# Kernel tuning notes

Measured on AMD Instinct MI355X. Metric: run time of the kernel, lower is better.

Reference implementation:

```python
import jax, jax.numpy as jnp
import numpy as np

# Router hyperparameters (from init_kwargs)
E = 64        # num_routed_experts
K = 6         # moe_router_topk
G = 8         # num_expert_groups
TG = 3        # topk_group
ALPHA = 0.001 # aux_loss_alpha
EPG = E // G  # experts per group


def setup_inputs() -> dict:
    key = jax.random.key(0)
    k1, k2 = jax.random.split(key)
    hidden_states = jax.random.normal(k1, (4, 4096, 4096), dtype=jnp.float32)
    # kaiming_uniform-ish scale for the gate weight [E, H]
    bound = 1.0 / np.sqrt(4096)
    weight = jax.random.uniform(k2, (E, 4096), dtype=jnp.float32,
                                minval=-bound, maxval=bound)
    return {"hidden_states": hidden_states, "weight": weight}


def reference(hidden_states, weight):
    B, S, H = hidden_states.shape
    T = B * S
    x = hidden_states.reshape(T, H).astype(jnp.float32)
    # gate GEMM + softmax scoring
    logits = jnp.einsum('th,eh->te', x, weight.astype(jnp.float32))  # [T, E]
    scores = jax.nn.softmax(logits, axis=-1)
    # group-limited greedy: keep only experts in the top-TG groups (by group max)
    group_scores = scores.reshape(T, G, EPG).max(axis=-1)            # [T, G]
    _, group_idx = jax.lax.top_k(group_scores, TG)                   # [T, TG]
    group_mask = jnp.zeros((T, G), scores.dtype).at[
        jnp.arange(T)[:, None], group_idx].set(1.0)                  # [T, G]
    score_mask = jnp.repeat(group_mask, EPG, axis=-1)                # [T, E]
    tmp_scores = jnp.where(score_mask > 0, scores, 0.0)
    topk_weight, topk_idx = jax.lax.top_k(tmp_scores, K)             # [T, K]
    # norm_topk_prob = True and top_k > 1 -> normalize
    topk_weight = topk_weight / (topk_weight.sum(axis=-1, keepdims=True) + 1e-20)
    # sequence-level aux loss (seq_aux=True, training, alpha > 0)
    idx_aux = topk_idx.reshape(B, S * K)                             # [B, S*K]
    ce = jax.vmap(lambda idx: jnp.zeros(E, jnp.float32).at[idx].add(1.0))(idx_aux)
    ce = ce / (S * K / E)                                            # [B, E]
    aux_loss = (ce * scores.reshape(B, S, E).mean(axis=1)).sum(axis=1).mean() * ALPHA
    return topk_idx, topk_weight, aux_loss
```

## Files before the change

### kernel.cpp

```cpp
#include <hip/hip_runtime.h>
#include <math.h>

#define TTOK   16384
#define HDIM   4096
#define ENUM   64
#define KTOP   6
#define GNUM   8
#define TGK    3
#define BBATCH 4
#define SSEQ   4096
#define ALPHAC 0.001f

#define KSPLIT 4
#define KSL    (HDIM / KSPLIT)
#define BK     64
#define GNIT   (KSL / BK)

#define AS3(p) ((__attribute__((address_space(3))) void*)(p))
#define AS1(p) ((const __attribute__((address_space(1))) void*)(p))

__global__ __launch_bounds__(256)
void pack_w(const float* __restrict__ W, float* __restrict__ Wp) {
    const int gid = blockIdx.x * 256 + threadIdx.x;
    const int k4 = gid >> 6, e = gid & 63;
    float4 v = *(const float4*)(W + (size_t)e * HDIM + k4 * 4);
    *(float4*)(Wp + (size_t)gid * 4) = v;
}

__global__ __launch_bounds__(512, 4)
void gate_gemm(const float* __restrict__ X, const float* __restrict__ Wp,
               float* __restrict__ lp) {
    __shared__ __align__(16) float Xs[2][64 * 64];

    const int tid = threadIdx.x;
    const int w   = __builtin_amdgcn_readfirstlane(tid >> 6);
    const int l   = tid & 63;
    const int tile  = blockIdx.x & 255;
    const int slice = blockIdx.x >> 8;
    const int tok0  = tile * 64;
    const int k0    = slice * KSL;

    const int t0 = w * 8 + (l >> 4);
    const int t1 = t0 + 4;
    const int q0 = (l & 15) ^ (t0 & 15);
    const int q1 = (l & 15) ^ (t1 & 15);
    const float* g0 = X + (size_t)(tok0 + t0) * HDIM + k0 + q0 * 4;
    const float* g1 = X + (size_t)(tok0 + t1) * HDIM + k0 + q1 * 4;

    float acc[8];
#pragma unroll
    for (int j = 0; j < 8; ++j) acc[j] = 0.f;

    const float4* Wp4 = (const float4*)Wp;
    const int k4base  = k0 >> 2;
    const int w8      = w * 8;
    const int lm      = (l & 15);

    __builtin_amdgcn_global_load_lds(AS1(g0), AS3(&Xs[0][w * 512 + 0]),   16, 0, 0);
    __builtin_amdgcn_global_load_lds(AS1(g1), AS3(&Xs[0][w * 512 + 256]), 16, 0, 0);

    for (int it = 0; it < GNIT; ++it) {
        __syncthreads();
        if (it + 1 < GNIT) {
            const int buf = (it + 1) & 1;
            const size_t go = (size_t)(it + 1) * BK;
            __builtin_amdgcn_global_load_lds(AS1(g0 + go), AS3(&Xs[buf][w * 512 + 0]),   16, 0, 0);
            __builtin_amdgcn_global_load_lds(AS1(g1 + go), AS3(&Xs[buf][w * 512 + 256]), 16, 0, 0);
        }
        const float* xb = &Xs[it & 1][l * 64];
        const int k4it  = k4base + it * 16;
#pragma unroll
        for (int kq = 0; kq < 16; ++kq) {
            const float4 xv = *(const float4*)(xb + ((kq ^ lm) << 2));
            const size_t wb = (size_t)(k4it + kq) * 64 + w8;
#pragma unroll
            for (int j = 0; j < 8; ++j) {
                const float4 wv = Wp4[wb + j];
                acc[j] = fmaf(xv.x, wv.x, acc[j]);
                acc[j] = fmaf(xv.y, wv.y, acc[j]);
                acc[j] = fmaf(xv.z, wv.z, acc[j]);
                acc[j] = fmaf(xv.w, wv.w, acc[j]);
            }
        }
    }

    float* dst = lp + (size_t)slice * TTOK * ENUM + (size_t)(tok0 + l) * ENUM + w8;
    *(float4*)(dst + 0) = make_float4(acc[0], acc[1], acc[2], acc[3]);
    *(float4*)(dst + 4) = make_float4(acc[4], acc[5], acc[6], acc[7]);
}

#define RTOK 64
__global__ __launch_bounds__(256)
void router_topk(const float* __restrict__ lp,
                 float* __restrict__ out_idx, float* __restrict__ out_w,
                 float* __restrict__ ssum_g, int* __restrict__ cnt_g) {
    __shared__ float Ls[RTOK * 67];
    __shared__ float s_m[RTOK], s_inv[RTOK];
    __shared__ float s_ssum[ENUM];
    __shared__ int   s_cnt[ENUM];

    const int tid = threadIdx.x;
    const int t0  = blockIdx.x * RTOK;
    if (tid < ENUM) { s_cnt[tid] = 0; s_ssum[tid] = 0.f; }

#pragma unroll
    for (int r = 0; r < 4; ++r) {
        const int q  = r * 256 + tid;
        const int t  = q >> 4, c4 = q & 15;
        const size_t base = (size_t)(t0 + t) * ENUM + c4 * 4;
        float4 v = *(const float4*)(lp + base);
#pragma unroll
        for (int h = 1; h < KSPLIT; ++h) {
            float4 u = *(const float4*)(lp + (size_t)h * TTOK * ENUM + base);
            v.x += u.x; v.y += u.y; v.z += u.z; v.w += u.w;
        }
        float* d = Ls + t * 67 + c4 * 4;
        d[0] = v.x; d[1] = v.y; d[2] = v.z; d[3] = v.w;
    }
    __syncthreads();

    if (tid < RTOK) {
        const float* row = Ls + tid * 67;

        float gm[GNUM];
#pragma unroll
        for (int g = 0; g < GNUM; ++g) {
            float mg = row[g * 8];
#pragma unroll
            for (int j = 1; j < 8; ++j) mg = fmaxf(mg, row[g * 8 + j]);
            gm[g] = mg;
        }
        float m = gm[0];
#pragma unroll
        for (int g = 1; g < GNUM; ++g) m = fmaxf(m, gm[g]);

        int selmask = 0;
#pragma unroll
        for (int g = 0; g < GNUM; ++g) {
            int rank = 0;
#pragma unroll
            for (int g2 = 0; g2 < GNUM; ++g2)
                rank += (gm[g2] > gm[g]) || (gm[g2] == gm[g] && g2 < g);
            selmask |= (rank < TGK) << g;
        }

        float v0=-1.f,v1=-1.f,v2=-1.f,v3=-1.f,v4=-1.f,v5=-1.f;
        float i0=0.f,i1=0.f,i2=0.f,i3=0.f,i4=0.f,i5=0.f;
        float s = 0.f;
#pragma unroll
        for (int e = 0; e < ENUM; ++e) {
            const float ex = __expf(row[e] - m);
            s += ex;
            const float cand = ((selmask >> (e >> 3)) & 1) ? ex : -1.0f;
            const float fe = (float)e;
            const bool b0 = cand > v0, b1 = cand > v1, b2 = cand > v2,
                       b3 = cand > v3, b4 = cand > v4, b5 = cand > v5;
            v5 = b4 ? v4 : (b5 ? cand : v5);  i5 = b4 ? i4 : (b5 ? fe : i5);
            v4 = b3 ? v3 : (b4 ? cand : v4);  i4 = b3 ? i3 : (b4 ? fe : i4);
            v3 = b2 ? v2 : (b3 ? cand : v3);  i3 = b2 ? i2 : (b3 ? fe : i3);
            v2 = b1 ? v1 : (b2 ? cand : v2);  i2 = b1 ? i1 : (b2 ? fe : i2);
            v1 = b0 ? v0 : (b1 ? cand : v1);  i1 = b0 ? i0 : (b1 ? fe : i1);
            v0 = b0 ? cand : v0;              i0 = b0 ? fe : i0;
        }
        const float invw = 1.0f / (v0 + v1 + v2 + v3 + v4 + v5);
        const int t = t0 + tid;
        float* oi = out_idx + (size_t)t * KTOP;
        float* ow = out_w   + (size_t)t * KTOP;
        oi[0]=i0; oi[1]=i1; oi[2]=i2; oi[3]=i3; oi[4]=i4; oi[5]=i5;
        ow[0]=v0*invw; ow[1]=v1*invw; ow[2]=v2*invw;
        ow[3]=v3*invw; ow[4]=v4*invw; ow[5]=v5*invw;

        atomicAdd(&s_cnt[(int)i0], 1); atomicAdd(&s_cnt[(int)i1], 1);
        atomicAdd(&s_cnt[(int)i2], 1); atomicAdd(&s_cnt[(int)i3], 1);
        atomicAdd(&s_cnt[(int)i4], 1); atomicAdd(&s_cnt[(int)i5], 1);
        s_m[tid] = m; s_inv[tid] = 1.0f / s;
    }
    __syncthreads();

    {
        const int e = tid & 63, strip = tid >> 6;
        float acc = 0.f;
#pragma unroll
        for (int i = 0; i < RTOK / 4; ++i) {
            const int t = strip * (RTOK / 4) + i;
            acc += __expf(Ls[t * 67 + e] - s_m[t]) * s_inv[t];
        }
        atomicAdd(&s_ssum[e], acc);
    }
    __syncthreads();

    const int b = t0 / SSEQ;
    if (tid < ENUM) {
        atomicAdd(&ssum_g[b * ENUM + tid], s_ssum[tid]);
        atomicAdd(&cnt_g[b * ENUM + tid], s_cnt[tid]);
    }
}

__global__ __launch_bounds__(256)
void aux_loss(const float* __restrict__ ssum_g, const int* __restrict__ cnt_g,
              float* __restrict__ out_aux) {
    const int tid = threadIdx.x;
    float v = (float)cnt_g[tid] * (float)ENUM / ((float)SSEQ * (float)KTOP)
            * (ssum_g[tid] / (float)SSEQ);
#pragma unroll
    for (int off = 32; off; off >>= 1) v += __shfl_xor(v, off);
    __shared__ float red[4];
    if ((tid & 63) == 0) red[tid >> 6] = v;
    __syncthreads();
    if (tid == 0)
        out_aux[0] = (red[0] + red[1] + red[2] + red[3]) * (ALPHAC / (float)BBATCH);
}

extern "C" void kernel_launch(void* const* d_in, const int* in_sizes, int n_in,
                              void* d_out, int out_size, void* d_ws, size_t ws_size,
                              hipStream_t stream) {
    const float* X = (const float*)d_in[0];
    const float* W = (const float*)d_in[1];

    float* out     = (float*)d_out;
    float* out_idx = out;
    float* out_w   = out + (size_t)TTOK * KTOP;
    float* out_aux = out + (size_t)2 * TTOK * KTOP;

    float* lp     = (float*)d_ws;
    float* Wp     = lp + (size_t)KSPLIT * TTOK * ENUM;
    float* ssum_g = Wp + (size_t)HDIM * ENUM;
    int*   cnt_g  = (int*)(ssum_g + BBATCH * ENUM);

    hipMemsetAsync(ssum_g, 0, BBATCH * ENUM * (sizeof(float) + sizeof(int)), stream);

    pack_w<<<(HDIM / 4) * ENUM / 256, 256, 0, stream>>>(W, Wp);
    gate_gemm<<<256 * KSPLIT, 512, 0, stream>>>(X, Wp, lp);
    router_topk<<<TTOK / RTOK, 256, 0, stream>>>(lp, out_idx, out_w, ssum_g, cnt_g);
    aux_loss<<<1, 256, 0, stream>>>(ssum_g, cnt_g, out_aux);
}
```

Before: 498.1 us.

## Retile gate GEMM to 256-token by 32-expert blocks with register blocking

Each block of the gate GEMM now covers 256 tokens and half of the experts, with BK set to 32. Each thread accumulates a 4x4 register tile of tokens by experts and loads a 16-float vector of W that is reused across 4 X rows. Blocks are remapped so that related blocks land on the same XCD. This cuts W load traffic per FMA, but X is now read twice from global memory, once per expert half.

```diff
diff --git a/kernel.cpp b/kernel.cpp
--- a/kernel.cpp
+++ b/kernel.cpp
@@ -13,11 +13,15 @@
 
 #define KSPLIT 4
 #define KSL    (HDIM / KSPLIT)
-#define BK     64
-#define GNIT   (KSL / BK)
+#define TM     256
+#define TE     32
+#define BK     32
+#define NIT    (KSL / BK)
 
 #define AS3(p) ((__attribute__((address_space(3))) void*)(p))
 #define AS1(p) ((const __attribute__((address_space(1))) void*)(p))
+
+typedef float wvec16 __attribute__((ext_vector_type(16)));
 
 __global__ __launch_bounds__(256)
 void pack_w(const float* __restrict__ W, float* __restrict__ Wp) {
@@ -30,63 +34,76 @@
 __global__ __launch_bounds__(512, 4)
 void gate_gemm(const float* __restrict__ X, const float* __restrict__ Wp,
                float* __restrict__ lp) {
-    __shared__ __align__(16) float Xs[2][64 * 64];
+    __shared__ __align__(16) float Xs[2][TM * BK];
 
     const int tid = threadIdx.x;
     const int w   = __builtin_amdgcn_readfirstlane(tid >> 6);
     const int l   = tid & 63;
-    const int tile  = blockIdx.x & 255;
-    const int slice = blockIdx.x >> 8;
-    const int tok0  = tile * 64;
-    const int k0    = slice * KSL;
-
-    const int t0 = w * 8 + (l >> 4);
-    const int t1 = t0 + 4;
-    const int q0 = (l & 15) ^ (t0 & 15);
-    const int q1 = (l & 15) ^ (t1 & 15);
-    const float* g0 = X + (size_t)(tok0 + t0) * HDIM + k0 + q0 * 4;
-    const float* g1 = X + (size_t)(tok0 + t1) * HDIM + k0 + q1 * 4;
-
-    float acc[8];
-#pragma unroll
-    for (int j = 0; j < 8; ++j) acc[j] = 0.f;
-
-    const float4* Wp4 = (const float4*)Wp;
-    const int k4base  = k0 >> 2;
-    const int w8      = w * 8;
-    const int lm      = (l & 15);
-
-    __builtin_amdgcn_global_load_lds(AS1(g0), AS3(&Xs[0][w * 512 + 0]),   16, 0, 0);
-    __builtin_amdgcn_global_load_lds(AS1(g1), AS3(&Xs[0][w * 512 + 256]), 16, 0, 0);
-
-    for (int it = 0; it < GNIT; ++it) {
+    const int lm7 = l & 7;
+
+    const int id     = blockIdx.x;
+    const int linear = (id & 7) * 64 + (id >> 3);
+    const int eh     = linear & 1;
+    const int ts     = linear >> 1;
+    const int tile   = ts & 63;
+    const int slice  = ts >> 6;
+    const int T0     = tile * TM;
+    const int k0     = slice * KSL;
+    const int E0     = eh * TE + w * 4;
+
+    const int trow = l >> 3;
+    const int kswz = ((l & 7) ^ trow) << 2;
+    const float* gs = X + (size_t)(T0 + w * 8 + trow) * HDIM + k0 + kswz;
+
+#define STAGE(buf_, it_) do {                                                   \
+    const size_t go_ = (size_t)(it_) * BK;                                      \
+    _Pragma("unroll")                                                           \
+    for (int r_ = 0; r_ < 4; ++r_)                                              \
+        __builtin_amdgcn_global_load_lds(                                       \
+            AS1(gs + (size_t)r_ * 64 * HDIM + go_),                             \
+            AS3(&Xs[buf_][r_ * 2048 + w * 256]), 16, 0, 0);                     \
+} while (0)
+
+    float acc[4][4];
+#pragma unroll
+    for (int g = 0; g < 4; ++g)
+#pragma unroll
+        for (int j = 0; j < 4; ++j) acc[g][j] = 0.f;
+
+    const int k4base = k0 >> 2;
+
+    STAGE(0, 0);
+
+    for (int it = 0; it < NIT; ++it) {
         __syncthreads();
-        if (it + 1 < GNIT) {
-            const int buf = (it + 1) & 1;
-            const size_t go = (size_t)(it + 1) * BK;
-            __builtin_amdgcn_global_load_lds(AS1(g0 + go), AS3(&Xs[buf][w * 512 + 0]),   16, 0, 0);
-            __builtin_amdgcn_global_load_lds(AS1(g1 + go), AS3(&Xs[buf][w * 512 + 256]), 16, 0, 0);
-        }
-        const float* xb = &Xs[it & 1][l * 64];
-        const int k4it  = k4base + it * 16;
-#pragma unroll
-        for (int kq = 0; kq < 16; ++kq) {
-            const float4 xv = *(const float4*)(xb + ((kq ^ lm) << 2));
-            const size_t wb = (size_t)(k4it + kq) * 64 + w8;
-#pragma unroll
-            for (int j = 0; j < 8; ++j) {
-                const float4 wv = Wp4[wb + j];
-                acc[j] = fmaf(xv.x, wv.x, acc[j]);
-                acc[j] = fmaf(xv.y, wv.y, acc[j]);
-                acc[j] = fmaf(xv.z, wv.z, acc[j]);
-                acc[j] = fmaf(xv.w, wv.w, acc[j]);
+        if (it + 1 < NIT) STAGE((it + 1) & 1, it + 1);
+
+        const float* xb = Xs[it & 1];
+        const int k4it  = k4base + it * (BK / 4);
+#pragma unroll
+        for (int kq = 0; kq < 8; ++kq) {
+            const wvec16 wv = *(const wvec16*)(Wp + ((size_t)(k4it + kq) * ENUM + E0) * 4);
+            const int slot = (kq ^ lm7) << 2;
+#pragma unroll
+            for (int g = 0; g < 4; ++g) {
+                const float4 xv = *(const float4*)(xb + (g * 64 + l) * BK + slot);
+#pragma unroll
+                for (int j = 0; j < 4; ++j) {
+                    acc[g][j] = fmaf(xv.x, wv[4 * j + 0], acc[g][j]);
+                    acc[g][j] = fmaf(xv.y, wv[4 * j + 1], acc[g][j]);
+                    acc[g][j] = fmaf(xv.z, wv[4 * j + 2], acc[g][j]);
+                    acc[g][j] = fmaf(xv.w, wv[4 * j + 3], acc[g][j]);
+                }
             }
         }
     }
 
-    float* dst = lp + (size_t)slice * TTOK * ENUM + (size_t)(tok0 + l) * ENUM + w8;
-    *(float4*)(dst + 0) = make_float4(acc[0], acc[1], acc[2], acc[3]);
-    *(float4*)(dst + 4) = make_float4(acc[4], acc[5], acc[6], acc[7]);
+    float* dst = lp + (size_t)slice * TTOK * ENUM + (size_t)(T0 + l) * ENUM + E0;
+#pragma unroll
+    for (int g = 0; g < 4; ++g)
+        *(float4*)(dst + (size_t)g * 64 * ENUM) =
+            make_float4(acc[g][0], acc[g][1], acc[g][2], acc[g][3]);
+#undef STAGE
 }
 
 #define RTOK 64
@@ -230,7 +247,7 @@
     hipMemsetAsync(ssum_g, 0, BBATCH * ENUM * (sizeof(float) + sizeof(int)), stream);
 
     pack_w<<<(HDIM / 4) * ENUM / 256, 256, 0, stream>>>(W, Wp);
-    gate_gemm<<<256 * KSPLIT, 512, 0, stream>>>(X, Wp, lp);
+    gate_gemm<<<512, 512, 0, stream>>>(X, Wp, lp);
     router_topk<<<TTOK / RTOK, 256, 0, stream>>>(lp, out_idx, out_w, ssum_g, cnt_g);
     aux_loss<<<1, 256, 0, stream>>>(ssum_g, cnt_g, out_aux);
 }
```

Result: faster. 424.0 us (-14.9%).
